# Kernel optimization log

Measured on AMD Instinct MI355X. Metric: run time of the kernel, lower is better.

## Reference

```python
import jax, jax.numpy as jnp
import numpy as np

B, N, T, J = 64, 64, 32, 128   # batch, num_hnodes, time_win, feature dim
IN_F, OUT_F = 4096, 256


def setup_inputs() -> dict:
    key = jax.random.key(0)
    k1, k2, k3 = jax.random.split(key, 3)
    inp = jax.random.normal(k1, (B, T, J, N), dtype=jnp.float32)
    indices = jax.random.randint(k2, (B, N, T), 0, IN_F, dtype=jnp.int64)
    full_weight = jax.random.normal(k3, (OUT_F, IN_F), dtype=jnp.float32)
    return {"input": inp, "indices": indices, "full_weight": full_weight}


def reference(input, indices, full_weight):
    # Gather columns of full_weight per (b, n, t): [OUT_F, B, N, T]
    w = full_weight[:, indices]
    # einsum 'bijk,lbki->bijl' with i=time, j=feat, k=hnodes, l=out
    y = jnp.einsum('btjn,lbnt->btjl', input, w)
    return y
```

## Files before the change

kernel.cpp:

```cpp
#include <hip/hip_runtime.h>
#include <hip/hip_bf16.h>
#include <stdint.h>

#define Bv   64
#define Tv   32
#define Jv   128
#define Nv   64
#define Lv   256
#define INFv 4096

typedef __attribute__((ext_vector_type(8))) short  short8;
typedef __attribute__((ext_vector_type(4))) float  floatx4;

__device__ __forceinline__ unsigned int f2bf(float f) {
  union { float f; unsigned int u; } v; v.f = f;
  unsigned int r = v.u + 0x7fffu + ((v.u >> 16) & 1u);
  return r >> 16;
}

__global__ __launch_bounds__(256) void wt_transpose_kernel(
    const float* __restrict__ w, unsigned short* __restrict__ wt) {
  int i_base = blockIdx.x * 16;
  int wave = threadIdx.x >> 6;
  int lane = threadIdx.x & 63;
  #pragma unroll
  for (int r = 0; r < 4; ++r) {
    int i = i_base + wave * 4 + r;
    unsigned int b0 = f2bf(w[(size_t)(4 * lane + 0) * INFv + i]);
    unsigned int b1 = f2bf(w[(size_t)(4 * lane + 1) * INFv + i]);
    unsigned int b2 = f2bf(w[(size_t)(4 * lane + 2) * INFv + i]);
    unsigned int b3 = f2bf(w[(size_t)(4 * lane + 3) * INFv + i]);
    uint2 u;
    u.x = b0 | (b1 << 16);
    u.y = b2 | (b3 << 16);
    *(uint2*)(wt + (size_t)i * Lv + 4 * lane) = u;
  }
}

__global__ __launch_bounds__(256, 2) void masklin_kernel(
    const float* __restrict__ x, const int* __restrict__ idx,
    const unsigned short* __restrict__ wt, const float* __restrict__ wfull,
    int use_wt, float* __restrict__ y) {
  __shared__ __align__(16) unsigned short lA[Jv * Nv];
  __shared__ __align__(16) unsigned short lB[Lv * Nv];
  __shared__ int idxs[Nv];

  int bt = blockIdx.x;
  int b = bt >> 5, t = bt & 31;
  int tid = threadIdx.x;
  int wave = tid >> 6, lane = tid & 63;

  if (tid < Nv) idxs[tid] = idx[(b * Nv + tid) * Tv + t];

  const float* xt = x + (size_t)(b * Tv + t) * (Jv * Nv);
  #pragma unroll
  for (int it = 0; it < 4; ++it) {
    int O = tid + it * 256;
    int j = O >> 3, c = O & 7;
    const float4* p = (const float4*)(xt + (size_t)O * 8);
    float4 a0 = p[0], a1 = p[1];
    uint4 v;
    v.x = f2bf(a0.x) | (f2bf(a0.y) << 16);
    v.y = f2bf(a0.z) | (f2bf(a0.w) << 16);
    v.z = f2bf(a1.x) | (f2bf(a1.y) << 16);
    v.w = f2bf(a1.z) | (f2bf(a1.w) << 16);
    *(uint4*)&lA[j * 64 + ((c ^ (j & 7)) << 3)] = v;
  }
  __syncthreads();

  {
    int l = tid;
    #pragma unroll
    for (int c = 0; c < 8; ++c) {
      unsigned int e[8];
      #pragma unroll
      for (int jj = 0; jj < 8; ++jj) {
        int n = c * 8 + jj;
        int in_row = idxs[n];
        if (use_wt) {
          e[jj] = wt[(size_t)in_row * Lv + l];
        } else {
          e[jj] = f2bf(wfull[(size_t)l * INFv + in_row]);
        }
      }
      uint4 v;
      v.x = e[0] | (e[1] << 16);
      v.y = e[2] | (e[3] << 16);
      v.z = e[4] | (e[5] << 16);
      v.w = e[6] | (e[7] << 16);
      *(uint4*)&lB[l * 64 + ((c ^ (l & 7)) << 3)] = v;
    }
  }
  __syncthreads();

  int m = lane & 15, qd = lane >> 4;
  floatx4 acc[8][4];
  #pragma unroll
  for (int jt = 0; jt < 8; ++jt)
    #pragma unroll
    for (int lt = 0; lt < 4; ++lt)
      acc[jt][lt] = (floatx4){0.f, 0.f, 0.f, 0.f};

  #pragma unroll
  for (int ks = 0; ks < 2; ++ks) {
    int chunk = ks * 4 + qd;
    short8 afr[8], bfr[4];
    #pragma unroll
    for (int jt = 0; jt < 8; ++jt) {
      int j = jt * 16 + m;
      afr[jt] = *(const short8*)&lA[j * 64 + ((chunk ^ (j & 7)) << 3)];
    }
    #pragma unroll
    for (int lt = 0; lt < 4; ++lt) {
      int l = wave * 64 + lt * 16 + m;
      bfr[lt] = *(const short8*)&lB[l * 64 + ((chunk ^ (l & 7)) << 3)];
    }
    #pragma unroll
    for (int jt = 0; jt < 8; ++jt)
      #pragma unroll
      for (int lt = 0; lt < 4; ++lt)
        acc[jt][lt] = __builtin_amdgcn_mfma_f32_16x16x32_bf16(
            afr[jt], bfr[lt], acc[jt][lt], 0, 0, 0);
  }

  float* yt = y + (size_t)(b * Tv + t) * (Jv * Lv);
  #pragma unroll
  for (int jt = 0; jt < 8; ++jt) {
    #pragma unroll
    for (int r = 0; r < 4; ++r) {
      int j = jt * 16 + qd * 4 + r;
      #pragma unroll
      for (int lt = 0; lt < 4; ++lt) {
        int l = wave * 64 + lt * 16 + m;
        yt[(size_t)j * Lv + l] = acc[jt][lt][r];
      }
    }
  }
}

extern "C" void kernel_launch(void* const* d_in, const int* in_sizes, int n_in,
                              void* d_out, int out_size, void* d_ws, size_t ws_size,
                              hipStream_t stream) {
  const float* x    = (const float*)d_in[0];
  const int*   idx  = (const int*)d_in[1];
  const float* w    = (const float*)d_in[2];
  float*       y    = (float*)d_out;

  const size_t wt_bytes = (size_t)INFv * Lv * sizeof(unsigned short);
  int use_wt = (d_ws != nullptr && ws_size >= wt_bytes) ? 1 : 0;
  unsigned short* wt = (unsigned short*)d_ws;

  if (use_wt) {
    wt_transpose_kernel<<<256, 256, 0, stream>>>(w, wt);
  }
  masklin_kernel<<<Bv * Tv, 256, 0, stream>>>(x, idx, wt, w, use_wt, y);
}
```

Baseline: 334.1 us.

## Load MFMA fragments directly from global, drop LDS, split J across two blocks

The kernel no longer stages operands in shared memory. Each lane loads its bf16 weight fragment (gathered rows) and input fragment straight into registers. Outputs are swapped so that each lane writes contiguous float4 runs with nontemporal stores. The grid is doubled by splitting J in half, the occupancy hint goes to 3 blocks, and use_wt becomes a template parameter. The goal is to remove LDS traffic and barriers and to get coalesced vector stores, at the cost of duplicated weight gathers across the two J halves and less coalesced fragment loads from global.

```diff
diff --git a/kernel.cpp b/kernel.cpp
--- a/kernel.cpp
+++ b/kernel.cpp
@@ -1,5 +1,4 @@
 #include <hip/hip_runtime.h>
-#include <hip/hip_bf16.h>
 #include <stdint.h>
 
 #define Bv   64
@@ -37,50 +36,45 @@
   }
 }
 
-__global__ __launch_bounds__(256, 2) void masklin_kernel(
+template <int USE_WT>
+__global__ __launch_bounds__(256, 3) void masklin_kernel(
     const float* __restrict__ x, const int* __restrict__ idx,
     const unsigned short* __restrict__ wt, const float* __restrict__ wfull,
-    int use_wt, float* __restrict__ y) {
-  __shared__ __align__(16) unsigned short lA[Jv * Nv];
-  __shared__ __align__(16) unsigned short lB[Lv * Nv];
-  __shared__ int idxs[Nv];
+    float* __restrict__ y) {
+  const int blk  = blockIdx.x;
+  const int bt   = blk >> 1;
+  const int jh   = blk & 1;
+  const int b    = bt >> 5;
+  const int t    = bt & 31;
+  const int tid  = threadIdx.x;
+  const int wave = tid >> 6;
+  const int lane = tid & 63;
+  const int m    = lane & 15;
+  const int qd   = lane >> 4;
+  const int lbase = wave << 6;
+  const int jbase = jh << 6;
 
-  int bt = blockIdx.x;
-  int b = bt >> 5, t = bt & 31;
-  int tid = threadIdx.x;
-  int wave = tid >> 6, lane = tid & 63;
+  const int* idxp = idx + ((b << 6) * Tv) + t;
+  int rows[16];
+  #pragma unroll
+  for (int ks = 0; ks < 2; ++ks)
+    #pragma unroll
+    for (int j = 0; j < 8; ++j)
+      rows[ks * 8 + j] = idxp[((ks << 5) + (qd << 3) + j) * Tv];
 
-  if (tid < Nv) idxs[tid] = idx[(b * Nv + tid) * Tv + t];
-
-  const float* xt = x + (size_t)(b * Tv + t) * (Jv * Nv);
+  short8 afr[2][4];
   #pragma unroll
-  for (int it = 0; it < 4; ++it) {
-    int O = tid + it * 256;
-    int j = O >> 3, c = O & 7;
-    const float4* p = (const float4*)(xt + (size_t)O * 8);
-    float4 a0 = p[0], a1 = p[1];
-    uint4 v;
-    v.x = f2bf(a0.x) | (f2bf(a0.y) << 16);
-    v.y = f2bf(a0.z) | (f2bf(a0.w) << 16);
-    v.z = f2bf(a1.x) | (f2bf(a1.y) << 16);
-    v.w = f2bf(a1.z) | (f2bf(a1.w) << 16);
-    *(uint4*)&lA[j * 64 + ((c ^ (j & 7)) << 3)] = v;
-  }
-  __syncthreads();
-
-  {
-    int l = tid;
+  for (int ks = 0; ks < 2; ++ks) {
     #pragma unroll
-    for (int c = 0; c < 8; ++c) {
+    for (int lt = 0; lt < 4; ++lt) {
+      const int lcol = lbase + (lt << 4) + m;
       unsigned int e[8];
       #pragma unroll
-      for (int jj = 0; jj < 8; ++jj) {
-        int n = c * 8 + jj;
-        int in_row = idxs[n];
-        if (use_wt) {
-          e[jj] = wt[(size_t)in_row * Lv + l];
+      for (int j = 0; j < 8; ++j) {
+        if (USE_WT) {
+          e[j] = wt[(unsigned int)rows[ks * 8 + j] * Lv + lcol];
         } else {
-          e[jj] = f2bf(wfull[(size_t)l * INFv + in_row]);
+          e[j] = f2bf(wfull[(size_t)lcol * INFv + rows[ks * 8 + j]]);
         }
       }
       uint4 v;
@@ -88,53 +82,51 @@
       v.y = e[2] | (e[3] << 16);
       v.z = e[4] | (e[5] << 16);
       v.w = e[6] | (e[7] << 16);
-      *(uint4*)&lB[l * 64 + ((c ^ (l & 7)) << 3)] = v;
+      afr[ks][lt] = *(short8*)&v;
     }
   }
-  __syncthreads();
 
-  int m = lane & 15, qd = lane >> 4;
-  floatx4 acc[8][4];
+  const float* xt = x + (size_t)bt * (Jv * Nv) + (size_t)jbase * Nv;
+  short8 bfr[2][4];
   #pragma unroll
-  for (int jt = 0; jt < 8; ++jt)
+  for (int jt = 0; jt < 4; ++jt) {
+    const float* xp = xt + (size_t)((jt << 4) + m) * Nv + (qd << 3);
+    #pragma unroll
+    for (int ks = 0; ks < 2; ++ks) {
+      float4 a0 = *(const float4*)(xp + (ks << 5));
+      float4 a1 = *(const float4*)(xp + (ks << 5) + 4);
+      uint4 v;
+      v.x = f2bf(a0.x) | (f2bf(a0.y) << 16);
+      v.y = f2bf(a0.z) | (f2bf(a0.w) << 16);
+      v.z = f2bf(a1.x) | (f2bf(a1.y) << 16);
+      v.w = f2bf(a1.z) | (f2bf(a1.w) << 16);
+      bfr[ks][jt] = *(short8*)&v;
+    }
+  }
+
+  floatx4 acc[4][4];
+  #pragma unroll
+  for (int lt = 0; lt < 4; ++lt)
+    #pragma unroll
+    for (int jt = 0; jt < 4; ++jt)
+      acc[lt][jt] = (floatx4){0.f, 0.f, 0.f, 0.f};
+
+  #pragma unroll
+  for (int ks = 0; ks < 2; ++ks)
+    #pragma unroll
+    for (int jt = 0; jt < 4; ++jt)
+      #pragma unroll
+      for (int lt = 0; lt < 4; ++lt)
+        acc[lt][jt] = __builtin_amdgcn_mfma_f32_16x16x32_bf16(
+            afr[ks][lt], bfr[ks][jt], acc[lt][jt], 0, 0, 0);
+
+  float* yt = y + (size_t)bt * (Jv * Lv);
+  #pragma unroll
+  for (int jt = 0; jt < 4; ++jt) {
+    float* yr = yt + (size_t)(jbase + (jt << 4) + m) * Lv + lbase + (qd << 2);
     #pragma unroll
     for (int lt = 0; lt < 4; ++lt)
-      acc[jt][lt] = (floatx4){0.f, 0.f, 0.f, 0.f};
-
-  #pragma unroll
-  for (int ks = 0; ks < 2; ++ks) {
-    int chunk = ks * 4 + qd;
-    short8 afr[8], bfr[4];
-    #pragma unroll
-    for (int jt = 0; jt < 8; ++jt) {
-      int j = jt * 16 + m;
-      afr[jt] = *(const short8*)&lA[j * 64 + ((chunk ^ (j & 7)) << 3)];
-    }
-    #pragma unroll
-    for (int lt = 0; lt < 4; ++lt) {
-      int l = wave * 64 + lt * 16 + m;
-      bfr[lt] = *(const short8*)&lB[l * 64 + ((chunk ^ (l & 7)) << 3)];
-    }
-    #pragma unroll
-    for (int jt = 0; jt < 8; ++jt)
-      #pragma unroll
-      for (int lt = 0; lt < 4; ++lt)
-        acc[jt][lt] = __builtin_amdgcn_mfma_f32_16x16x32_bf16(
-            afr[jt], bfr[lt], acc[jt][lt], 0, 0, 0);
-  }
-
-  float* yt = y + (size_t)(b * Tv + t) * (Jv * Lv);
-  #pragma unroll
-  for (int jt = 0; jt < 8; ++jt) {
-    #pragma unroll
-    for (int r = 0; r < 4; ++r) {
-      int j = jt * 16 + qd * 4 + r;
-      #pragma unroll
-      for (int lt = 0; lt < 4; ++lt) {
-        int l = wave * 64 + lt * 16 + m;
-        yt[(size_t)j * Lv + l] = acc[jt][lt][r];
-      }
-    }
+      __builtin_nontemporal_store(acc[lt][jt], (floatx4*)(yr + (lt << 4)));
   }
 }
 
@@ -152,6 +144,8 @@
 
   if (use_wt) {
     wt_transpose_kernel<<<256, 256, 0, stream>>>(w, wt);
+    masklin_kernel<1><<<Bv * Tv * 2, 256, 0, stream>>>(x, idx, wt, w, y);
+  } else {
+    masklin_kernel<0><<<Bv * Tv * 2, 256, 0, stream>>>(x, idx, (const unsigned short*)nullptr, w, y);
   }
-  masklin_kernel<<<Bv * Tv, 256, 0, stream>>>(x, idx, wt, w, use_wt, y);
 }
```

Result: slower. 360.2 us (+7.8%).
